# Optimization experiments

Measured on AMD Instinct MI355X. Metric: run time of the kernel, lower is better.

## Reference

```python
import jax, jax.numpy as jnp
import numpy as np


def setup_inputs() -> dict:
    key = jax.random.key(0)
    k1, k2 = jax.random.split(key)
    N, M, D = 8192, 8192, 128
    z_anc = jax.random.normal(k1, (N, D), dtype=jnp.float32)
    z_pos_neg = jax.random.normal(k2, (M, D), dtype=jnp.float32)
    return {"z_anc": z_anc, "z_pos_neg": z_pos_neg}


def reference(z_anc, z_pos_neg):
    # -||a_i - b_j||_2 computed via the GEMM expansion
    # ||a-b||^2 = ||a||^2 + ||b||^2 - 2 a.b  (avoids the O(N*M*D) broadcast)
    a2 = jnp.sum(z_anc * z_anc, axis=-1)          # [N]
    b2 = jnp.sum(z_pos_neg * z_pos_neg, axis=-1)  # [M]
    ab = jnp.einsum("nd,md->nm", z_anc, z_pos_neg)  # [N, M]
    d2 = jnp.maximum(a2[:, None] + b2[None, :] - 2.0 * ab, 0.0)
    return -jnp.sqrt(d2)
```

## Files before the change

### kernel.cpp

```cpp
#include <hip/hip_runtime.h>
#include <hip/hip_bf16.h>

#define D_DIM 128
#define TILE 128
#define LDS_K (D_DIM + 8)

typedef __attribute__((ext_vector_type(8))) short short8;
typedef __attribute__((ext_vector_type(4))) float floatx4;

__global__ void prep_kernel(const float* __restrict__ za, const float* __restrict__ zb,
                            __hip_bfloat16* __restrict__ abf, __hip_bfloat16* __restrict__ bbf,
                            float* __restrict__ a2, float* __restrict__ b2, int N) {
    int r = blockIdx.x * 4 + (threadIdx.x >> 6);
    int lane = threadIdx.x & 63;
    const float* src; __hip_bfloat16* dst; float* nrm; int row;
    if (r < N) { src = za; dst = abf; nrm = a2; row = r; }
    else       { src = zb; dst = bbf; nrm = b2; row = r - N; }
    const float2 v = ((const float2*)(src + (size_t)row * D_DIM))[lane];
    __hip_bfloat16 h0 = __float2bfloat16(v.x);
    __hip_bfloat16 h1 = __float2bfloat16(v.y);
    float f0 = __bfloat162float(h0), f1 = __bfloat162float(h1);
    float ss = f0 * f0 + f1 * f1;
    ushort2 st;
    st.x = *(const unsigned short*)&h0;
    st.y = *(const unsigned short*)&h1;
    ((ushort2*)(dst + (size_t)row * D_DIM))[lane] = st;
    #pragma unroll
    for (int off = 32; off; off >>= 1) ss += __shfl_down(ss, off, 64);
    if (lane == 0) nrm[row] = ss;
}

__global__ __launch_bounds__(256, 2)
void dist_kernel(const __hip_bfloat16* __restrict__ abf, const __hip_bfloat16* __restrict__ bbf,
                 const float* __restrict__ a2, const float* __restrict__ b2,
                 float* __restrict__ out, int M) {
    __shared__ __hip_bfloat16 As[TILE][LDS_K];
    __shared__ __hip_bfloat16 Bs[TILE][LDS_K];

    const int rowBase = blockIdx.y * TILE;
    const int colBase = blockIdx.x * TILE;
    const int tid = threadIdx.x;

    #pragma unroll
    for (int pass = 0; pass < 8; ++pass) {
        int idx = pass * 256 + tid;
        int row = idx >> 4;
        int kc  = (idx & 15) * 8;
        uint4 va = *(const uint4*)(abf + ((size_t)(rowBase + row) * D_DIM + kc));
        *(uint4*)(&As[row][kc]) = va;
        uint4 vb = *(const uint4*)(bbf + ((size_t)(colBase + row) * D_DIM + kc));
        *(uint4*)(&Bs[row][kc]) = vb;
    }
    __syncthreads();

    const int wave = tid >> 6;
    const int lane = tid & 63;
    const int wr = (wave >> 1) * 64;
    const int wc = (wave & 1) * 64;
    const int lrow = lane & 15;
    const int lk = (lane >> 4) * 8;

    floatx4 acc[4][4] = {};
    #pragma unroll
    for (int ks = 0; ks < 4; ++ks) {
        const int k0 = ks * 32 + lk;
        short8 afr[4], bfr[4];
        #pragma unroll
        for (int i = 0; i < 4; ++i)
            afr[i] = *(const short8*)(&As[wr + i * 16 + lrow][k0]);
        #pragma unroll
        for (int j = 0; j < 4; ++j)
            bfr[j] = *(const short8*)(&Bs[wc + j * 16 + lrow][k0]);
        #pragma unroll
        for (int i = 0; i < 4; ++i)
            #pragma unroll
            for (int j = 0; j < 4; ++j)
                acc[i][j] = __builtin_amdgcn_mfma_f32_16x16x32_bf16(afr[i], bfr[j], acc[i][j], 0, 0, 0);
    }

    const int crow0 = rowBase + wr + (lane >> 4) * 4;
    const int ccol0 = colBase + wc + lrow;
    #pragma unroll
    for (int i = 0; i < 4; ++i) {
        #pragma unroll
        for (int r = 0; r < 4; ++r) {
            const int n = crow0 + i * 16 + r;
            const float an = a2[n];
            const size_t rowOff = (size_t)n * (size_t)M;
            #pragma unroll
            for (int j = 0; j < 4; ++j) {
                const int m = ccol0 + j * 16;
                float d2 = an + b2[m] - 2.0f * acc[i][j][r];
                d2 = fmaxf(d2, 0.0f);
                out[rowOff + m] = -sqrtf(d2);
            }
        }
    }
}

extern "C" void kernel_launch(void* const* d_in, const int* in_sizes, int n_in,
                              void* d_out, int out_size, void* d_ws, size_t ws_size,
                              hipStream_t stream) {
    const float* za = (const float*)d_in[0];
    const float* zb = (const float*)d_in[1];
    const int N = in_sizes[0] / D_DIM;
    const int M = in_sizes[1] / D_DIM;
    float* out = (float*)d_out;

    char* ws = (char*)d_ws;
    __hip_bfloat16* abf = (__hip_bfloat16*)ws;
    __hip_bfloat16* bbf = (__hip_bfloat16*)(ws + (size_t)N * D_DIM * sizeof(__hip_bfloat16));
    float* a2 = (float*)(ws + (size_t)(N + M) * D_DIM * sizeof(__hip_bfloat16));
    float* b2 = a2 + N;

    prep_kernel<<<(N + M) / 4, 256, 0, stream>>>(za, zb, abf, bbf, a2, b2, N);

    dim3 grid(M / TILE, N / TILE);
    dist_kernel<<<grid, 256, 0, stream>>>(abf, bbf, a2, b2, out, M);
}
```

Baseline: 280.9 us.

## Fuse bf16 conversion and norms into dist kernel, swap MFMA operands for vector stores

Removes the separate prep kernel. Each tile block now loads fp32 inputs, converts them to bf16 in LDS, and computes squared norms in shared memory. The MFMA operand roles are swapped so each lane's four accumulator values are contiguous along the output column, which enables float4 stores. It also uses the fast amdgcn sqrt. This saves a launch and the workspace round trip, but every block re-converts its tiles, so fp32 global reads double and the conversion is repeated redundantly across 64 blocks per row tile.

```diff
diff --git a/kernel.cpp b/kernel.cpp
--- a/kernel.cpp
+++ b/kernel.cpp
@@ -8,55 +8,52 @@
 typedef __attribute__((ext_vector_type(8))) short short8;
 typedef __attribute__((ext_vector_type(4))) float floatx4;
 
-__global__ void prep_kernel(const float* __restrict__ za, const float* __restrict__ zb,
-                            __hip_bfloat16* __restrict__ abf, __hip_bfloat16* __restrict__ bbf,
-                            float* __restrict__ a2, float* __restrict__ b2, int N) {
-    int r = blockIdx.x * 4 + (threadIdx.x >> 6);
-    int lane = threadIdx.x & 63;
-    const float* src; __hip_bfloat16* dst; float* nrm; int row;
-    if (r < N) { src = za; dst = abf; nrm = a2; row = r; }
-    else       { src = zb; dst = bbf; nrm = b2; row = r - N; }
-    const float2 v = ((const float2*)(src + (size_t)row * D_DIM))[lane];
-    __hip_bfloat16 h0 = __float2bfloat16(v.x);
-    __hip_bfloat16 h1 = __float2bfloat16(v.y);
-    float f0 = __bfloat162float(h0), f1 = __bfloat162float(h1);
-    float ss = f0 * f0 + f1 * f1;
-    ushort2 st;
-    st.x = *(const unsigned short*)&h0;
-    st.y = *(const unsigned short*)&h1;
-    ((ushort2*)(dst + (size_t)row * D_DIM))[lane] = st;
-    #pragma unroll
-    for (int off = 32; off; off >>= 1) ss += __shfl_down(ss, off, 64);
-    if (lane == 0) nrm[row] = ss;
-}
-
 __global__ __launch_bounds__(256, 2)
-void dist_kernel(const __hip_bfloat16* __restrict__ abf, const __hip_bfloat16* __restrict__ bbf,
-                 const float* __restrict__ a2, const float* __restrict__ b2,
+void dist_kernel(const float* __restrict__ za, const float* __restrict__ zb,
                  float* __restrict__ out, int M) {
     __shared__ __hip_bfloat16 As[TILE][LDS_K];
     __shared__ __hip_bfloat16 Bs[TILE][LDS_K];
+    __shared__ alignas(16) float a2s[TILE];
+    __shared__ alignas(16) float b2s[TILE];
 
-    const int rowBase = blockIdx.y * TILE;
-    const int colBase = blockIdx.x * TILE;
+    const int nBase = blockIdx.y * TILE;
+    const int mBase = blockIdx.x * TILE;
     const int tid = threadIdx.x;
+    const int lane = tid & 63;
 
     #pragma unroll
-    for (int pass = 0; pass < 8; ++pass) {
-        int idx = pass * 256 + tid;
-        int row = idx >> 4;
-        int kc  = (idx & 15) * 8;
-        uint4 va = *(const uint4*)(abf + ((size_t)(rowBase + row) * D_DIM + kc));
-        *(uint4*)(&As[row][kc]) = va;
-        uint4 vb = *(const uint4*)(bbf + ((size_t)(colBase + row) * D_DIM + kc));
-        *(uint4*)(&Bs[row][kc]) = vb;
+    for (int pass = 0; pass < 16; ++pass) {
+        const bool isA = pass < 8;
+        const int idx = (pass & 7) * 256 + tid;
+        const int row = idx >> 4;
+        const int kc = (idx & 15) * 8;
+        const float* src = isA ? (za + ((size_t)(nBase + row) * D_DIM + kc))
+                               : (zb + ((size_t)(mBase + row) * D_DIM + kc));
+        const float4 v0 = ((const float4*)src)[0];
+        const float4 v1 = ((const float4*)src)[1];
+        __hip_bfloat16 h[8];
+        h[0] = __float2bfloat16(v0.x); h[1] = __float2bfloat16(v0.y);
+        h[2] = __float2bfloat16(v0.z); h[3] = __float2bfloat16(v0.w);
+        h[4] = __float2bfloat16(v1.x); h[5] = __float2bfloat16(v1.y);
+        h[6] = __float2bfloat16(v1.z); h[7] = __float2bfloat16(v1.w);
+        short8 pk;
+        float ss = 0.0f;
+        #pragma unroll
+        for (int t = 0; t < 8; ++t) {
+            pk[t] = (short)__builtin_bit_cast(unsigned short, h[t]);
+            const float f = __bfloat162float(h[t]);
+            ss = fmaf(f, f, ss);
+        }
+        *(short8*)(isA ? &As[row][kc] : &Bs[row][kc]) = pk;
+        #pragma unroll
+        for (int off = 1; off < 16; off <<= 1) ss += __shfl_xor(ss, off, 64);
+        if ((lane & 15) == 0) (isA ? a2s : b2s)[row] = ss;
     }
     __syncthreads();
 
     const int wave = tid >> 6;
-    const int lane = tid & 63;
-    const int wr = (wave >> 1) * 64;
-    const int wc = (wave & 1) * 64;
+    const int wm = (wave & 1) * 64;
+    const int wn = (wave >> 1) * 64;
     const int lrow = lane & 15;
     const int lk = (lane >> 4) * 8;
 
@@ -64,36 +61,45 @@
     #pragma unroll
     for (int ks = 0; ks < 4; ++ks) {
         const int k0 = ks * 32 + lk;
-        short8 afr[4], bfr[4];
+        short8 mfr[4], nfr[4];
         #pragma unroll
         for (int i = 0; i < 4; ++i)
-            afr[i] = *(const short8*)(&As[wr + i * 16 + lrow][k0]);
+            mfr[i] = *(const short8*)(&Bs[wm + i * 16 + lrow][k0]);
         #pragma unroll
         for (int j = 0; j < 4; ++j)
-            bfr[j] = *(const short8*)(&Bs[wc + j * 16 + lrow][k0]);
+            nfr[j] = *(const short8*)(&As[wn + j * 16 + lrow][k0]);
         #pragma unroll
         for (int i = 0; i < 4; ++i)
             #pragma unroll
             for (int j = 0; j < 4; ++j)
-                acc[i][j] = __builtin_amdgcn_mfma_f32_16x16x32_bf16(afr[i], bfr[j], acc[i][j], 0, 0, 0);
+                acc[i][j] = __builtin_amdgcn_mfma_f32_16x16x32_bf16(mfr[i], nfr[j], acc[i][j], 0, 0, 0);
     }
 
-    const int crow0 = rowBase + wr + (lane >> 4) * 4;
-    const int ccol0 = colBase + wc + lrow;
+    const int mLoc = wm + (lane >> 4) * 4;
+    const int nLoc0 = wn + lrow;
+
+    float4 b2v[4];
     #pragma unroll
-    for (int i = 0; i < 4; ++i) {
+    for (int i = 0; i < 4; ++i)
+        b2v[i] = *(const float4*)(&b2s[mLoc + i * 16]);
+
+    #pragma unroll
+    for (int j = 0; j < 4; ++j) {
+        const int n = nBase + nLoc0 + j * 16;
+        const float an = a2s[nLoc0 + j * 16];
+        float* orow = out + (size_t)n * (size_t)M + mBase;
         #pragma unroll
-        for (int r = 0; r < 4; ++r) {
-            const int n = crow0 + i * 16 + r;
-            const float an = a2[n];
-            const size_t rowOff = (size_t)n * (size_t)M;
-            #pragma unroll
-            for (int j = 0; j < 4; ++j) {
-                const int m = ccol0 + j * 16;
-                float d2 = an + b2[m] - 2.0f * acc[i][j][r];
-                d2 = fmaxf(d2, 0.0f);
-                out[rowOff + m] = -sqrtf(d2);
-            }
+        for (int i = 0; i < 4; ++i) {
+            float4 v;
+            const float d2x = fmaxf(fmaf(-2.0f, acc[i][j][0], an + b2v[i].x), 0.0f);
+            const float d2y = fmaxf(fmaf(-2.0f, acc[i][j][1], an + b2v[i].y), 0.0f);
+            const float d2z = fmaxf(fmaf(-2.0f, acc[i][j][2], an + b2v[i].z), 0.0f);
+            const float d2w = fmaxf(fmaf(-2.0f, acc[i][j][3], an + b2v[i].w), 0.0f);
+            v.x = -__builtin_amdgcn_sqrtf(d2x);
+            v.y = -__builtin_amdgcn_sqrtf(d2y);
+            v.z = -__builtin_amdgcn_sqrtf(d2z);
+            v.w = -__builtin_amdgcn_sqrtf(d2w);
+            *(float4*)(orow + mLoc + i * 16) = v;
         }
     }
 }
@@ -107,14 +113,6 @@
     const int M = in_sizes[1] / D_DIM;
     float* out = (float*)d_out;
 
-    char* ws = (char*)d_ws;
-    __hip_bfloat16* abf = (__hip_bfloat16*)ws;
-    __hip_bfloat16* bbf = (__hip_bfloat16*)(ws + (size_t)N * D_DIM * sizeof(__hip_bfloat16));
-    float* a2 = (float*)(ws + (size_t)(N + M) * D_DIM * sizeof(__hip_bfloat16));
-    float* b2 = a2 + N;
-
-    prep_kernel<<<(N + M) / 4, 256, 0, stream>>>(za, zb, abf, bbf, a2, b2, N);
-
     dim3 grid(M / TILE, N / TILE);
-    dist_kernel<<<grid, 256, 0, stream>>>(abf, bbf, a2, b2, out, M);
+    dist_kernel<<<grid, 256, 0, stream>>>(za, zb, out, M);
 }
```

After: 345.6 us. 23.0% more time.
